# Kernel optimization log

Measured on AMD Instinct MI355X. Metric: run time of the kernel, lower is better.

## Reference

```python
import jax, jax.numpy as jnp
import numpy as np

N, E, DIM, H = 50000, 800000, 128, 8
HD = DIM // H  # head_dim = 16
HID = 4 * DIM  # ffn hidden (hidden_dim_multiplier=4)


def setup_inputs() -> dict:
    key = jax.random.key(0)
    ks = jax.random.split(key, 12)
    s = 0.05
    return {
        "x": jax.random.normal(ks[0], (N, DIM), jnp.float32),
        "src": jax.random.randint(ks[1], (E,), 0, N, jnp.int32),
        "dst": jax.random.randint(ks[2], (E,), 0, N, jnp.int32),
        "fc_w": jax.random.normal(ks[3], (DIM, DIM), jnp.float32) * s,
        "fc_b": jax.random.normal(ks[4], (DIM,), jnp.float32) * s,
        "au_w": jax.random.normal(ks[5], (H, DIM), jnp.float32) * s,
        "au_b": jax.random.normal(ks[6], (H,), jnp.float32) * s,
        "av_w": jax.random.normal(ks[7], (H, DIM), jnp.float32) * s,
        "w1": jax.random.normal(ks[8], (HID, 4 * DIM), jnp.float32) * s,
        "b1": jax.random.normal(ks[9], (HID,), jnp.float32) * s,
        "w2": jax.random.normal(ks[10], (DIM, HID), jnp.float32) * s,
        "b2": jax.random.normal(ks[11], (DIM,), jnp.float32) * s,
    }


def reference(x, src, dst, fc_w, fc_b, au_w, au_b, av_w, w1, b1, w2, b2):
    h = x @ fc_w.T + fc_b                                   # [N, DIM]
    su = h @ au_w.T + au_b                                  # [N, H]
    sv = h @ av_w.T                                         # [N, H] (no bias)
    # u_add_v + LeakyReLU(0.2)
    scores = jax.nn.leaky_relu(su[src] + sv[dst], 0.2)      # [E, H]
    # edge_softmax grouped by destination node (stable)
    m = jax.ops.segment_max(scores, dst, num_segments=N)    # [N, H]
    ex = jnp.exp(scores - m[dst])
    den = jax.ops.segment_sum(ex, dst, num_segments=N)      # [N, H]
    probs = ex / den[dst]                                   # [E, H]
    # u_mul_e_sum over heads: x reshaped [N, head_dim, H]
    xh = h.reshape(N, HD, H)
    msg = jax.ops.segment_sum(xh[src] * probs[:, None, :], dst, num_segments=N)
    msg = msg.reshape(N, DIM)
    # copy_u_mean: mean of src features over incoming edges
    ones = jnp.ones((E,), h.dtype)
    in_deg = jax.ops.segment_sum(ones, dst, num_segments=N)   # [N]
    sum2 = jax.ops.segment_sum(xh[src], dst, num_segments=N)  # [N, HD, H]
    msg2 = (sum2 / jnp.maximum(in_deg, 1.0)[:, None, None]).reshape(N, DIM)
    # symmetric-norm message: norm = 1/sqrt(out_deg[src]*out_deg[dst])
    out_deg = jax.ops.segment_sum(ones, src, num_segments=N)  # [N]
    norm = 1.0 / jnp.sqrt(out_deg[src] * out_deg[dst])        # [E]
    msg3 = jax.ops.segment_sum(h[src] * norm[:, None], dst, num_segments=N)
    # combine + feed-forward (dropout=0 -> identity)
    cat = jnp.concatenate([h, msg, msg2, msg3], axis=1)       # [N, 4*DIM]
    f = jax.nn.gelu(cat @ w1.T + b1, approximate=False)
    return f @ w2.T + b2                                      # [N, DIM]
```

## Files before the change

kernel.cpp:

```cpp
#include <hip/hip_runtime.h>
#include <hip/hip_bf16.h>

#define NNODES 50000
#define NEDGES 800000
#define DIM 128
#define NH 8
#define HID 512
#define NB 196

typedef unsigned short ushort_t;
typedef unsigned int uint_t;
typedef __attribute__((ext_vector_type(8))) short bf16x8;
typedef __attribute__((ext_vector_type(4))) float f32x4;

__device__ __forceinline__ ushort_t f2bf_bits(float v) {
    __hip_bfloat16 b = __float2bfloat16(v);
    return *(ushort_t*)&b;
}

__global__ __launch_bounds__(256) void convert_weights_kernel(
    const float* __restrict__ fc_w, const float* __restrict__ fc_b,
    const float* __restrict__ au_w, const float* __restrict__ au_b,
    const float* __restrict__ av_w,
    const float* __restrict__ w1, const float* __restrict__ w2,
    ushort_t* __restrict__ fc_wb, ushort_t* __restrict__ w1b,
    ushort_t* __restrict__ w2b,
    ushort_t* __restrict__ afc, float* __restrict__ abc)
{
    int i = blockIdx.x * 256 + threadIdx.x;
    if (i < 16384)
        ((__hip_bfloat16*)fc_wb)[i] = __float2bfloat16(fc_w[i]);
    else if (i < 278528)
        ((__hip_bfloat16*)w1b)[i - 16384] = __float2bfloat16(w1[i - 16384]);
    else if (i < 344064)
        ((__hip_bfloat16*)w2b)[i - 278528] = __float2bfloat16(w2[i - 278528]);

    if (i < 2048) {
        int row = i >> 7, col = i & 127;
        const float* wrow = (row < 8) ? (au_w + row * DIM) : (av_w + (row - 8) * DIM);
        float s = 0.f;
        for (int j = 0; j < DIM; ++j) s += wrow[j] * fc_w[j * DIM + col];
        afc[row * DIM + col] = f2bf_bits(s);
    }
    if (i < 16) {
        const float* wrow = (i < 8) ? (au_w + i * DIM) : (av_w + (i - 8) * DIM);
        float s = (i < 8) ? au_b[i] : 0.f;
        for (int j = 0; j < DIM; ++j) s += wrow[j] * fc_b[j];
        abc[i] = s;
    }
}

__global__ __launch_bounds__(256, 4) void fc_attn_kernel(
    const float* __restrict__ x,
    const ushort_t* __restrict__ fc_wb, const float* __restrict__ fc_b,
    const ushort_t* __restrict__ afc, const float* __restrict__ abc,
    ushort_t* __restrict__ hb, float* __restrict__ su, float* __restrict__ sv,
    int M)
{
    constexpr int PAD = 8;
    __shared__ ushort_t Ws[128][128 + PAD];
    __shared__ ushort_t Aw[16][128 + PAD];

    const int t    = threadIdx.x;
    const int wid  = t >> 6, lane = t & 63;
    const int qd   = lane >> 4, l16 = lane & 15;

#pragma unroll
    for (int i = 0; i < 8; ++i) {
        int v = t + i * 256;
        int row = v >> 4, ch = v & 15;
        *(uint4*)(&Ws[row][ch * 8]) = *(const uint4*)(fc_wb + row * 128 + ch * 8);
    }
    {
        int row = t >> 4, ch = t & 15;
        *(uint4*)(&Aw[row][ch * 8]) = *(const uint4*)(afc + row * 128 + ch * 8);
    }
    __syncthreads();

    const int tile = blockIdx.x * 4 + wid;
    if (tile * 16 >= M) return;

    const int arow = tile * 16 + l16;
    const float* xp = x + (size_t)arow * DIM + qd * 8;
    const float cb = abc[l16];

    f32x4 acc[8], accs;
#pragma unroll
    for (int i = 0; i < 8; ++i) acc[i] = (f32x4){0.f, 0.f, 0.f, 0.f};
    accs = (f32x4){0.f, 0.f, 0.f, 0.f};

#pragma unroll
    for (int ks = 0; ks < 4; ++ks) {
        float4 f0 = *(const float4*)(xp + ks * 32);
        float4 f1 = *(const float4*)(xp + ks * 32 + 4);
        union { ushort_t u[8]; bf16x8 v; } a;
        a.u[0] = f2bf_bits(f0.x); a.u[1] = f2bf_bits(f0.y);
        a.u[2] = f2bf_bits(f0.z); a.u[3] = f2bf_bits(f0.w);
        a.u[4] = f2bf_bits(f1.x); a.u[5] = f2bf_bits(f1.y);
        a.u[6] = f2bf_bits(f1.z); a.u[7] = f2bf_bits(f1.w);
#pragma unroll
        for (int nf = 0; nf < 8; ++nf) {
            bf16x8 bw = *(const bf16x8*)(&Ws[nf * 16 + l16][ks * 32 + qd * 8]);
            acc[nf] = __builtin_amdgcn_mfma_f32_16x16x32_bf16(a.v, bw, acc[nf], 0, 0, 0);
        }
        bf16x8 ba = *(const bf16x8*)(&Aw[l16][ks * 32 + qd * 8]);
        accs = __builtin_amdgcn_mfma_f32_16x16x32_bf16(a.v, ba, accs, 0, 0, 0);
    }

#pragma unroll
    for (int r = 0; r < 4; ++r) {
        int grow = tile * 16 + qd * 4 + r;
#pragma unroll
        for (int nf = 0; nf < 8; ++nf) {
            int gc = nf * 16 + l16;
            hb[(size_t)grow * DIM + gc] = f2bf_bits(acc[nf][r] + fc_b[gc]);
        }
        float vs = accs[r] + cb;
        if (l16 < 8) su[(size_t)grow * NH + l16] = vs;
        else         sv[(size_t)grow * NH + (l16 - 8)] = vs;
    }
}

__global__ __launch_bounds__(512, 4) void ffn_fused_kernel(
    const ushort_t* __restrict__ cat,
    const ushort_t* __restrict__ w1b,
    const float* __restrict__ b1,
    const ushort_t* __restrict__ w2b,
    const float* __restrict__ b2,
    float* __restrict__ out, int M)
{
    constexpr int BM = 128, BK = 32, PAD = 8;
    __shared__ ushort_t As[BM][BK + PAD];
    __shared__ ushort_t Bs[128][BK + PAD];
    __shared__ ushort_t Fs[128][128 + PAD];

    const int t    = threadIdx.x;
    const int bm   = blockIdx.x * BM;
    const int wid  = t >> 6, lane = t & 63;
    const int wrow = wid >> 2;
    const int wcol = wid & 3;
    const int qd   = lane >> 4, l16 = lane & 15;

    const int sr = t >> 2, sc8 = (t & 3) * 8;

    f32x4 acc_o[4][2];
#pragma unroll
    for (int i = 0; i < 4; ++i)
#pragma unroll
        for (int j = 0; j < 2; ++j) acc_o[i][j] = (f32x4){0.f, 0.f, 0.f, 0.f};

    for (int p = 0; p < 4; ++p) {
        f32x4 acc_f[4][2];
#pragma unroll
        for (int i = 0; i < 4; ++i)
#pragma unroll
            for (int j = 0; j < 2; ++j) acc_f[i][j] = (f32x4){0.f, 0.f, 0.f, 0.f};

        for (int k0 = 0; k0 < HID; k0 += BK) {
            {
                int gr = bm + sr;
                uint4 val = make_uint4(0u, 0u, 0u, 0u);
                if (gr < M) val = *(const uint4*)(cat + (size_t)gr * HID + k0 + sc8);
                *(uint4*)(&As[sr][sc8]) = val;
                *(uint4*)(&Bs[sr][sc8]) =
                    *(const uint4*)(w1b + (size_t)(p * 128 + sr) * HID + k0 + sc8);
            }
            __syncthreads();

            bf16x8 af[4], bfr[2];
#pragma unroll
            for (int mi = 0; mi < 4; ++mi)
                af[mi] = *(const bf16x8*)(&As[wrow * 64 + mi * 16 + l16][qd * 8]);
#pragma unroll
            for (int ni = 0; ni < 2; ++ni)
                bfr[ni] = *(const bf16x8*)(&Bs[wcol * 32 + ni * 16 + l16][qd * 8]);
#pragma unroll
            for (int mi = 0; mi < 4; ++mi)
#pragma unroll
                for (int ni = 0; ni < 2; ++ni)
                    acc_f[mi][ni] = __builtin_amdgcn_mfma_f32_16x16x32_bf16(
                        af[mi], bfr[ni], acc_f[mi][ni], 0, 0, 0);
            __syncthreads();
        }

#pragma unroll
        for (int mi = 0; mi < 4; ++mi) {
#pragma unroll
            for (int r = 0; r < 4; ++r) {
                int lrow = wrow * 64 + mi * 16 + qd * 4 + r;
#pragma unroll
                for (int ni = 0; ni < 2; ++ni) {
                    int lcol = wcol * 32 + ni * 16 + l16;
                    float v = acc_f[mi][ni][r] + b1[p * 128 + lcol];
                    v = 0.5f * v * (1.f + erff(v * 0.70710678118654752f));
                    Fs[lrow][lcol] = f2bf_bits(v);
                }
            }
        }
        __syncthreads();

#pragma unroll
        for (int kk = 0; kk < 4; ++kk) {
            bf16x8 af2[4], bf2[2];
#pragma unroll
            for (int mi = 0; mi < 4; ++mi)
                af2[mi] = *(const bf16x8*)(&Fs[wrow * 64 + mi * 16 + l16][kk * 32 + qd * 8]);
#pragma unroll
            for (int ni = 0; ni < 2; ++ni) {
                int col2 = wcol * 32 + ni * 16 + l16;
                bf2[ni] = *(const bf16x8*)(w2b + (size_t)col2 * HID + p * 128 + kk * 32 + qd * 8);
            }
#pragma unroll
            for (int mi = 0; mi < 4; ++mi)
#pragma unroll
                for (int ni = 0; ni < 2; ++ni)
                    acc_o[mi][ni] = __builtin_amdgcn_mfma_f32_16x16x32_bf16(
                        af2[mi], bf2[ni], acc_o[mi][ni], 0, 0, 0);
        }
        __syncthreads();
    }

#pragma unroll
    for (int mi = 0; mi < 4; ++mi) {
#pragma unroll
        for (int r = 0; r < 4; ++r) {
            int lrow = wrow * 64 + mi * 16 + qd * 4 + r;
            int grow = bm + lrow;
            if (grow >= M) continue;
#pragma unroll
            for (int ni = 0; ni < 2; ++ni) {
                int gc = wcol * 32 + ni * 16 + l16;
                out[(size_t)grow * DIM + gc] = acc_o[mi][ni][r] + b2[gc];
            }
        }
    }
}

__global__ __launch_bounds__(256) void degree_count_kernel(
    const int* __restrict__ src, const int* __restrict__ dst,
    float* __restrict__ out_deg, int* __restrict__ in_cnt, int E)
{
    int e = blockIdx.x * 256 + threadIdx.x;
    if (e >= E) return;
    unsafeAtomicAdd(&out_deg[src[e]], 1.f);
    atomicAdd(&in_cnt[dst[e]], 1);
}

__global__ __launch_bounds__(256) void block_sum_kernel(
    const int* __restrict__ cnt, int* __restrict__ bsum)
{
    const int lane = threadIdx.x & 63, wid = threadIdx.x >> 6;
    int i = blockIdx.x * 256 + threadIdx.x;
    int v = (i < NNODES) ? cnt[i] : 0;
#pragma unroll
    for (int off = 32; off >= 1; off >>= 1) v += __shfl_down(v, off, 64);
    __shared__ int ws_[4];
    if (lane == 0) ws_[wid] = v;
    __syncthreads();
    if (threadIdx.x == 0) bsum[blockIdx.x] = ws_[0] + ws_[1] + ws_[2] + ws_[3];
}

__global__ __launch_bounds__(256) void block_scan_kernel(
    const int* __restrict__ bsum, int* __restrict__ boff)
{
    __shared__ int sb[256];
    const int t = threadIdx.x;
    int v = (t < NB) ? bsum[t] : 0;
    sb[t] = v;
    __syncthreads();
    for (int off = 1; off < 256; off <<= 1) {
        int u = (t >= off) ? sb[t - off] : 0;
        __syncthreads();
        sb[t] += u;
        __syncthreads();
    }
    if (t < NB) boff[t] = (t == 0) ? 0 : sb[t - 1];
}

__global__ __launch_bounds__(256) void final_scan_kernel(
    const int* __restrict__ cnt, const int* __restrict__ boff,
    int* __restrict__ rowstart)
{
    __shared__ int sb[256];
    const int t = threadIdx.x;
    const int b = blockIdx.x;
    int i = b * 256 + t;
    int v = (i < NNODES) ? cnt[i] : 0;
    sb[t] = v;
    __syncthreads();
    for (int off = 1; off < 256; off <<= 1) {
        int u = (t >= off) ? sb[t - off] : 0;
        __syncthreads();
        sb[t] += u;
        __syncthreads();
    }
    if (i < NNODES) rowstart[i] = boff[b] + sb[t] - v;
    if (b == 0 && t == 0) rowstart[NNODES] = NEDGES;
}

__global__ __launch_bounds__(256) void fill_csr_kernel(
    const int* __restrict__ src, const int* __restrict__ dst,
    const int* __restrict__ rowstart, int* __restrict__ cursor,
    int* __restrict__ esrc, int E)
{
    int e = blockIdx.x * 256 + threadIdx.x;
    if (e >= E) return;
    int d = dst[e];
    int pos = rowstart[d] + atomicAdd(&cursor[d], 1);
    esrc[pos] = src[e];
}

__device__ __forceinline__ float bf_lo(uint_t v) {
    union { uint_t i; float f; } c; c.i = v << 16; return c.f;
}
__device__ __forceinline__ float bf_hi(uint_t v) {
    union { uint_t i; float f; } c; c.i = v & 0xffff0000u; return c.f;
}
__device__ __forceinline__ void st_bf2(ushort_t* p, float a, float b) {
    __hip_bfloat16 ba = __float2bfloat16(a), bb = __float2bfloat16(b);
    uint_t v = (uint_t)(*(ushort_t*)&ba) | ((uint_t)(*(ushort_t*)&bb) << 16);
    *(uint_t*)p = v;
}

__global__ __launch_bounds__(256) void gather_aggregate_kernel(
    const int* __restrict__ rowstart, const int* __restrict__ esrc,
    const ushort_t* __restrict__ hb,
    const float* __restrict__ su, const float* __restrict__ sv,
    const float* __restrict__ out_deg,
    ushort_t* __restrict__ cat, int N)
{
    const int wave = threadIdx.x >> 6;
    const int lane = threadIdx.x & 63;
    const int n = blockIdx.x * 4 + wave;
    if (n >= N) return;

    const int d0 = lane << 1;
    const int h0 = d0 & 7;

    const int e0  = rowstart[n];
    const int deg = rowstart[n + 1] - e0;
    const float2 svv = *(const float2*)(sv + (size_t)n * NH + h0);
    const float od_d = out_deg[n];

    int es = 0;
    if (deg > 0) es = esrc[e0 + (lane < deg ? lane : deg - 1)];

    float den0 = 0.f, den1 = 0.f;
    float m0 = 0.f, m1 = 0.f, s0 = 0.f, s1 = 0.f, n0 = 0.f, n1 = 0.f;

#define GA_LOADS(u, jj)                                                       \
    {                                                                         \
        int sv_ = ((jj) < 64) ? __shfl(es, (jj), 64) : esrc[e0 + (jj)];       \
        sX[u] = __builtin_amdgcn_readfirstlane(sv_);                          \
    }
#define GA_FETCH(u)                                                           \
    {                                                                         \
        suX[u] = *(const float2*)(su + (size_t)sX[u] * NH + h0);              \
        odX[u] = out_deg[sX[u]];                                              \
        hvX[u] = *(const uint_t*)(hb + (size_t)sX[u] * DIM + d0);             \
    }
#define GA_COMPUTE(u)                                                         \
    {                                                                         \
        float sc0 = suX[u].x + svv.x; sc0 = sc0 < 0.f ? 0.2f * sc0 : sc0;     \
        float sc1 = suX[u].y + svv.y; sc1 = sc1 < 0.f ? 0.2f * sc1 : sc1;     \
        float ex0 = __expf(sc0), ex1 = __expf(sc1);                           \
        den0 += ex0; den1 += ex1;                                             \
        float nrm = rsqrtf(odX[u] * od_d);                                    \
        float hs0 = bf_lo(hvX[u]), hs1 = bf_hi(hvX[u]);                       \
        m0 += hs0 * ex0; m1 += hs1 * ex1;                                     \
        s0 += hs0;       s1 += hs1;                                           \
        n0 += hs0 * nrm; n1 += hs1 * nrm;                                     \
    }

    int j = 0;
    const int deg8 = deg & ~7;
    for (; j < deg8; j += 8) {
        int sX[8]; float2 suX[8]; float odX[8]; uint_t hvX[8];
#pragma unroll
        for (int u = 0; u < 8; ++u) GA_LOADS(u, j + u)
#pragma unroll
        for (int u = 0; u < 8; ++u) GA_FETCH(u)
#pragma unroll
        for (int u = 0; u < 8; ++u) GA_COMPUTE(u)
    }
    if (deg & 4) {
        int sX[4]; float2 suX[4]; float odX[4]; uint_t hvX[4];
#pragma unroll
        for (int u = 0; u < 4; ++u) GA_LOADS(u, j + u)
#pragma unroll
        for (int u = 0; u < 4; ++u) GA_FETCH(u)
#pragma unroll
        for (int u = 0; u < 4; ++u) GA_COMPUTE(u)
        j += 4;
    }
    for (; j < deg; ++j) {
        int sX[1]; float2 suX[1]; float odX[1]; uint_t hvX[1];
        GA_LOADS(0, j)
        GA_FETCH(0)
        GA_COMPUTE(0)
    }
#undef GA_LOADS
#undef GA_FETCH
#undef GA_COMPUTE

    const float inv = 1.f / fmaxf((float)deg, 1.f);
    const float r0 = den0 > 0.f ? 1.f / den0 : 0.f;
    const float r1 = den1 > 0.f ? 1.f / den1 : 0.f;
    ushort_t* row = cat + (size_t)n * 512;
    *(uint_t*)(row + d0) = *(const uint_t*)(hb + (size_t)n * DIM + d0);
    st_bf2(row + 128 + d0, m0 * r0, m1 * r1);
    st_bf2(row + 256 + d0, s0 * inv, s1 * inv);
    st_bf2(row + 384 + d0, n0, n1);
}

extern "C" void kernel_launch(void* const* d_in, const int* in_sizes, int n_in,
                              void* d_out, int out_size, void* d_ws, size_t ws_size,
                              hipStream_t stream)
{
    const float* x    = (const float*)d_in[0];
    const int*   src  = (const int*)d_in[1];
    const int*   dst  = (const int*)d_in[2];
    const float* fc_w = (const float*)d_in[3];
    const float* fc_b = (const float*)d_in[4];
    const float* au_w = (const float*)d_in[5];
    const float* au_b = (const float*)d_in[6];
    const float* av_w = (const float*)d_in[7];
    const float* w1   = (const float*)d_in[8];
    const float* b1   = (const float*)d_in[9];
    const float* w2   = (const float*)d_in[10];
    const float* b2   = (const float*)d_in[11];
    float* out = (float*)d_out;

    const int N = NNODES, E = NEDGES;

    char* w = (char*)d_ws;
    ushort_t* fc_wb = (ushort_t*)w;  w += (size_t)DIM * DIM * 2;
    ushort_t* w1b   = (ushort_t*)w;  w += (size_t)HID * 512 * 2;
    ushort_t* w2b   = (ushort_t*)w;  w += (size_t)DIM * HID * 2;
    ushort_t* afc   = (ushort_t*)w;  w += (size_t)16 * DIM * 2;
    float* abc      = (float*)w;     w += (size_t)16 * 4;
    ushort_t* hb    = (ushort_t*)w;  w += (size_t)N * DIM * 2;
    ushort_t* cat   = (ushort_t*)w;  w += (size_t)N * 512 * 2;
    float* su       = (float*)w;     w += (size_t)N * NH * 4;
    float* sv       = (float*)w;     w += (size_t)N * NH * 4;
    float* out_deg  = (float*)w;     w += (size_t)N * 4;
    int*   in_cnt   = (int*)w;       w += (size_t)N * 4;
    int*   cursor   = (int*)w;       w += (size_t)N * 4;
    int*   rowstart = (int*)w;       w += (size_t)(N + 16) * 4;
    int*   bsum     = (int*)w;       w += (size_t)256 * 4;
    int*   boff     = (int*)w;       w += (size_t)256 * 4;
    int*   esrc     = (int*)w;       w += (size_t)E * 4;

    (void)hipMemsetAsync(out_deg, 0, (size_t)N * 3 * 4, stream);

    convert_weights_kernel<<<1344, 256, 0, stream>>>(
        fc_w, fc_b, au_w, au_b, av_w, w1, w2, fc_wb, w1b, w2b, afc, abc);

    fc_attn_kernel<<<(N / 16 + 3) / 4, 256, 0, stream>>>(
        x, fc_wb, fc_b, afc, abc, hb, su, sv, N);

    degree_count_kernel<<<(E + 255) / 256, 256, 0, stream>>>(src, dst, out_deg, in_cnt, E);
    block_sum_kernel<<<NB, 256, 0, stream>>>(in_cnt, bsum);
    block_scan_kernel<<<1, 256, 0, stream>>>(bsum, boff);
    final_scan_kernel<<<NB, 256, 0, stream>>>(in_cnt, boff, rowstart);
    fill_csr_kernel<<<(E + 255) / 256, 256, 0, stream>>>(src, dst, rowstart, cursor, esrc, E);
    gather_aggregate_kernel<<<(N + 3) / 4, 256, 0, stream>>>(
        rowstart, esrc, hb, su, sv, out_deg, cat, N);

    ffn_fused_kernel<<<(N + 127) / 128, 512, 0, stream>>>(
        cat, w1b, b1, w2b, b2, out, N);
}
```

Baseline: 372.1 us.

## Merge degree counting into weight conversion, fold block scan, use nontemporal memory ops

Degree counting now runs as extra blocks appended to the weight-conversion kernel. The separate single-block scan kernel is removed: each final-scan block sums the preceding block totals itself with a wave reduction. Nontemporal loads and stores are added for x, the cat buffer and the output. Together these cut two kernel launches and aim to reduce cache pollution from streamed data, at the cost of some redundant prefix summing per block and a possible loss of cache reuse for cat, which the FFN kernel reads several times.

```diff
diff --git a/kernel.cpp b/kernel.cpp
--- a/kernel.cpp
+++ b/kernel.cpp
@@ -7,27 +7,42 @@
 #define NH 8
 #define HID 512
 #define NB 196
+#define CVT_BLOCKS 1344
+#define DEG_BLOCKS 3125
 
 typedef unsigned short ushort_t;
 typedef unsigned int uint_t;
 typedef __attribute__((ext_vector_type(8))) short bf16x8;
 typedef __attribute__((ext_vector_type(4))) float f32x4;
+typedef __attribute__((ext_vector_type(4))) uint_t u32x4;
 
 __device__ __forceinline__ ushort_t f2bf_bits(float v) {
     __hip_bfloat16 b = __float2bfloat16(v);
     return *(ushort_t*)&b;
 }
 
-__global__ __launch_bounds__(256) void convert_weights_kernel(
+__global__ __launch_bounds__(256) void convert_deg_kernel(
     const float* __restrict__ fc_w, const float* __restrict__ fc_b,
     const float* __restrict__ au_w, const float* __restrict__ au_b,
     const float* __restrict__ av_w,
     const float* __restrict__ w1, const float* __restrict__ w2,
+    const int* __restrict__ src, const int* __restrict__ dst,
     ushort_t* __restrict__ fc_wb, ushort_t* __restrict__ w1b,
     ushort_t* __restrict__ w2b,
-    ushort_t* __restrict__ afc, float* __restrict__ abc)
-{
-    int i = blockIdx.x * 256 + threadIdx.x;
+    ushort_t* __restrict__ afc, float* __restrict__ abc,
+    float* __restrict__ out_deg, int* __restrict__ in_cnt, int E)
+{
+    const int b = blockIdx.x;
+    if (b >= CVT_BLOCKS) {
+        int e = (b - CVT_BLOCKS) * 256 + threadIdx.x;
+        if (e < E) {
+            unsafeAtomicAdd(&out_deg[src[e]], 1.f);
+            atomicAdd(&in_cnt[dst[e]], 1);
+        }
+        return;
+    }
+
+    int i = b * 256 + threadIdx.x;
     if (i < 16384)
         ((__hip_bfloat16*)fc_wb)[i] = __float2bfloat16(fc_w[i]);
     else if (i < 278528)
@@ -91,8 +106,8 @@
 
 #pragma unroll
     for (int ks = 0; ks < 4; ++ks) {
-        float4 f0 = *(const float4*)(xp + ks * 32);
-        float4 f1 = *(const float4*)(xp + ks * 32 + 4);
+        f32x4 f0 = __builtin_nontemporal_load((const f32x4*)(xp + ks * 32));
+        f32x4 f1 = __builtin_nontemporal_load((const f32x4*)(xp + ks * 32 + 4));
         union { ushort_t u[8]; bf16x8 v; } a;
         a.u[0] = f2bf_bits(f0.x); a.u[1] = f2bf_bits(f0.y);
         a.u[2] = f2bf_bits(f0.z); a.u[3] = f2bf_bits(f0.w);
@@ -159,11 +174,13 @@
         for (int k0 = 0; k0 < HID; k0 += BK) {
             {
                 int gr = bm + sr;
-                uint4 val = make_uint4(0u, 0u, 0u, 0u);
-                if (gr < M) val = *(const uint4*)(cat + (size_t)gr * HID + k0 + sc8);
-                *(uint4*)(&As[sr][sc8]) = val;
-                *(uint4*)(&Bs[sr][sc8]) =
-                    *(const uint4*)(w1b + (size_t)(p * 128 + sr) * HID + k0 + sc8);
+                u32x4 val = (u32x4){0u, 0u, 0u, 0u};
+                if (gr < M)
+                    val = __builtin_nontemporal_load(
+                        (const u32x4*)(cat + (size_t)gr * HID + k0 + sc8));
+                *(u32x4*)(&As[sr][sc8]) = val;
+                *(u32x4*)(&Bs[sr][sc8]) =
+                    *(const u32x4*)(w1b + (size_t)(p * 128 + sr) * HID + k0 + sc8);
             }
             __syncthreads();
 
@@ -230,20 +247,11 @@
 #pragma unroll
             for (int ni = 0; ni < 2; ++ni) {
                 int gc = wcol * 32 + ni * 16 + l16;
-                out[(size_t)grow * DIM + gc] = acc_o[mi][ni][r] + b2[gc];
+                __builtin_nontemporal_store(acc_o[mi][ni][r] + b2[gc],
+                                            out + (size_t)grow * DIM + gc);
             }
         }
     }
-}
-
-__global__ __launch_bounds__(256) void degree_count_kernel(
-    const int* __restrict__ src, const int* __restrict__ dst,
-    float* __restrict__ out_deg, int* __restrict__ in_cnt, int E)
-{
-    int e = blockIdx.x * 256 + threadIdx.x;
-    if (e >= E) return;
-    unsafeAtomicAdd(&out_deg[src[e]], 1.f);
-    atomicAdd(&in_cnt[dst[e]], 1);
 }
 
 __global__ __launch_bounds__(256) void block_sum_kernel(
@@ -260,30 +268,27 @@
     if (threadIdx.x == 0) bsum[blockIdx.x] = ws_[0] + ws_[1] + ws_[2] + ws_[3];
 }
 
-__global__ __launch_bounds__(256) void block_scan_kernel(
-    const int* __restrict__ bsum, int* __restrict__ boff)
+__global__ __launch_bounds__(256) void final_scan_kernel(
+    const int* __restrict__ cnt, const int* __restrict__ bsum,
+    int* __restrict__ rowstart)
 {
     __shared__ int sb[256];
-    const int t = threadIdx.x;
-    int v = (t < NB) ? bsum[t] : 0;
-    sb[t] = v;
-    __syncthreads();
-    for (int off = 1; off < 256; off <<= 1) {
-        int u = (t >= off) ? sb[t - off] : 0;
-        __syncthreads();
-        sb[t] += u;
-        __syncthreads();
-    }
-    if (t < NB) boff[t] = (t == 0) ? 0 : sb[t - 1];
-}
-
-__global__ __launch_bounds__(256) void final_scan_kernel(
-    const int* __restrict__ cnt, const int* __restrict__ boff,
-    int* __restrict__ rowstart)
-{
-    __shared__ int sb[256];
+    __shared__ int ws_[4];
+    __shared__ int basev;
     const int t = threadIdx.x;
     const int b = blockIdx.x;
+    const int lane = t & 63, wid = t >> 6;
+
+    {
+        int v = (t < b) ? bsum[t] : 0;
+#pragma unroll
+        for (int off = 32; off >= 1; off >>= 1) v += __shfl_down(v, off, 64);
+        if (lane == 0) ws_[wid] = v;
+        __syncthreads();
+        if (t == 0) basev = ws_[0] + ws_[1] + ws_[2] + ws_[3];
+        __syncthreads();
+    }
+
     int i = b * 256 + t;
     int v = (i < NNODES) ? cnt[i] : 0;
     sb[t] = v;
@@ -294,7 +299,7 @@
         sb[t] += u;
         __syncthreads();
     }
-    if (i < NNODES) rowstart[i] = boff[b] + sb[t] - v;
+    if (i < NNODES) rowstart[i] = basev + sb[t] - v;
     if (b == 0 && t == 0) rowstart[NNODES] = NEDGES;
 }
 
@@ -316,10 +321,10 @@
 __device__ __forceinline__ float bf_hi(uint_t v) {
     union { uint_t i; float f; } c; c.i = v & 0xffff0000u; return c.f;
 }
-__device__ __forceinline__ void st_bf2(ushort_t* p, float a, float b) {
+__device__ __forceinline__ void st_bf2_nt(ushort_t* p, float a, float b) {
     __hip_bfloat16 ba = __float2bfloat16(a), bb = __float2bfloat16(b);
     uint_t v = (uint_t)(*(ushort_t*)&ba) | ((uint_t)(*(ushort_t*)&bb) << 16);
-    *(uint_t*)p = v;
+    __builtin_nontemporal_store(v, (uint_t*)p);
 }
 
 __global__ __launch_bounds__(256) void gather_aggregate_kernel(
@@ -407,10 +412,11 @@
     const float r0 = den0 > 0.f ? 1.f / den0 : 0.f;
     const float r1 = den1 > 0.f ? 1.f / den1 : 0.f;
     ushort_t* row = cat + (size_t)n * 512;
-    *(uint_t*)(row + d0) = *(const uint_t*)(hb + (size_t)n * DIM + d0);
-    st_bf2(row + 128 + d0, m0 * r0, m1 * r1);
-    st_bf2(row + 256 + d0, s0 * inv, s1 * inv);
-    st_bf2(row + 384 + d0, n0, n1);
+    __builtin_nontemporal_store(*(const uint_t*)(hb + (size_t)n * DIM + d0),
+                                (uint_t*)(row + d0));
+    st_bf2_nt(row + 128 + d0, m0 * r0, m1 * r1);
+    st_bf2_nt(row + 256 + d0, s0 * inv, s1 * inv);
+    st_bf2_nt(row + 384 + d0, n0, n1);
 }
 
 extern "C" void kernel_launch(void* const* d_in, const int* in_sizes, int n_in,
@@ -453,17 +459,17 @@
 
     (void)hipMemsetAsync(out_deg, 0, (size_t)N * 3 * 4, stream);
 
-    convert_weights_kernel<<<1344, 256, 0, stream>>>(
-        fc_w, fc_b, au_w, au_b, av_w, w1, w2, fc_wb, w1b, w2b, afc, abc);
+    convert_deg_kernel<<<CVT_BLOCKS + DEG_BLOCKS, 256, 0, stream>>>(
+        fc_w, fc_b, au_w, au_b, av_w, w1, w2, src, dst,
+        fc_wb, w1b, w2b, afc, abc, out_deg, in_cnt, E);
 
     fc_attn_kernel<<<(N / 16 + 3) / 4, 256, 0, stream>>>(
         x, fc_wb, fc_b, afc, abc, hb, su, sv, N);
 
-    degree_count_kernel<<<(E + 255) / 256, 256, 0, stream>>>(src, dst, out_deg, in_cnt, E);
     block_sum_kernel<<<NB, 256, 0, stream>>>(in_cnt, bsum);
-    block_scan_kernel<<<1, 256, 0, stream>>>(bsum, boff);
-    final_scan_kernel<<<NB, 256, 0, stream>>>(in_cnt, boff, rowstart);
+    final_scan_kernel<<<NB, 256, 0, stream>>>(in_cnt, bsum, rowstart);
     fill_csr_kernel<<<(E + 255) / 256, 256, 0, stream>>>(src, dst, rowstart, cursor, esrc, E);
+
     gather_aggregate_kernel<<<(N + 3) / 4, 256, 0, stream>>>(
         rowstart, esrc, hb, su, sv, out_deg, cat, N);
 
```

Measured after the change: 395.4 us. 6.3% more time.
